# Performance work log

Measured on AMD Instinct MI355X. Metric: run time of the kernel, lower is better.

Reference implementation:

```python
import jax, jax.numpy as jnp
import numpy as np

D_MODEL = 1024
NUM_HEADS = 16
KEY_DIM = 64
VALUE_DIM = 64
NEG_INF = jnp.float32(-1e30)


def setup_inputs() -> dict:
    key = jax.random.key(0)
    ks = jax.random.split(key, 10)
    B, S = 2, 2048
    lim = 1.0 / np.sqrt(D_MODEL)
    x = jax.random.normal(ks[0], (B, S, D_MODEL), dtype=jnp.float32)
    mask = jnp.ones((B, S), dtype=jnp.int32)  # pad mask: 1 = keep
    # stacked per-head linear params (Linear stores weight as [out, in])
    Wq = jax.random.uniform(ks[1], (NUM_HEADS, KEY_DIM, D_MODEL), jnp.float32, -lim, lim)
    bq = jax.random.uniform(ks[2], (NUM_HEADS, KEY_DIM), jnp.float32, -lim, lim)
    Wk = jax.random.uniform(ks[3], (NUM_HEADS, KEY_DIM, D_MODEL), jnp.float32, -lim, lim)
    bk = jax.random.uniform(ks[4], (NUM_HEADS, KEY_DIM), jnp.float32, -lim, lim)
    Wv = jax.random.uniform(ks[5], (NUM_HEADS, VALUE_DIM, D_MODEL), jnp.float32, -lim, lim)
    bv = jax.random.uniform(ks[6], (NUM_HEADS, VALUE_DIM), jnp.float32, -lim, lim)
    lim_o = 1.0 / np.sqrt(NUM_HEADS * VALUE_DIM)
    Wo = jax.random.uniform(ks[7], (D_MODEL, NUM_HEADS * VALUE_DIM), jnp.float32, -lim_o, lim_o)
    bo = jax.random.uniform(ks[8], (D_MODEL,), jnp.float32, -lim_o, lim_o)
    return {"x": x, "mask": mask, "Wq": Wq, "bq": bq, "Wk": Wk, "bk": bk,
            "Wv": Wv, "bv": bv, "Wo": Wo, "bo": bo}


def _mha(x, mask, Wq, bq, Wk, bk, Wv, bv, Wo, bo):
    B, S, _ = x.shape
    # per-head projections: [B, H, S, k]
    q = jnp.einsum('bsd,hkd->bhsk', x, Wq) + bq[None, :, None, :]
    k = jnp.einsum('bsd,hkd->bhsk', x, Wk) + bk[None, :, None, :]
    v = jnp.einsum('bsd,hvd->bhsv', x, Wv) + bv[None, :, None, :]
    scale = 1.0 / np.sqrt(KEY_DIM).astype(np.float32)
    scores = jnp.einsum('bhik,bhjk->bhij', q, k) * scale  # [B, H, S, S]
    # final mask = causal AND pad-row AND pad-col
    causal = jnp.tril(jnp.ones((S, S), dtype=bool))
    pad = mask.astype(bool)
    final = causal[None, None] & pad[:, None, :, None] & pad[:, None, None, :]
    masked = jnp.where(final, scores, NEG_INF)
    w = jax.nn.softmax(masked, axis=-1)
    w = jnp.where(final, w, 0.0)  # fully-masked rows -> zeros, matching loop impl
    out = jnp.einsum('bhij,bhjv->bhiv', w, v)            # [B, H, S, V]
    concat = out.transpose(0, 2, 1, 3).reshape(B, S, NUM_HEADS * VALUE_DIM)
    return concat @ Wo.T + bo


def reference(x, mask, Wq, bq, Wk, bk, Wv, bv, Wo, bo):
    return _mha(x, mask, Wq, bq, Wk, bk, Wv, bv, Wo, bo)
```

## Files before the change

kernel.cpp:

```cpp
#include <hip/hip_runtime.h>

#define SEQ 2048
#define NH 16
#define HD 64
#define DMODEL 1024

__device__ __forceinline__ unsigned int f2bf(float f) {
  unsigned int u = __float_as_uint(f);
  return ((u + 0x7fffu + ((u >> 16) & 1u)) >> 16) & 0xffffu;
}

__device__ __forceinline__ unsigned int pk2bf(float a, float b) {
  unsigned short ua = __builtin_bit_cast(unsigned short, (__bf16)a);
  unsigned short ub = __builtin_bit_cast(unsigned short, (__bf16)b);
  return (unsigned int)ua | ((unsigned int)ub << 16);
}

typedef __bf16 bf16x8 __attribute__((ext_vector_type(8)));
typedef float f32x4 __attribute__((ext_vector_type(4)));

__device__ __forceinline__ void gl2lds16(const unsigned short* g, unsigned short* l) {
  __builtin_amdgcn_global_load_lds(
      (const __attribute__((address_space(1))) unsigned int*)g,
      (__attribute__((address_space(3))) unsigned int*)l, 16, 0, 0);
}

__global__ __launch_bounds__(256) void cast_all_kernel(
    const float* __restrict__ x, const float* __restrict__ wq,
    const float* __restrict__ wk, const float* __restrict__ wv,
    const float* __restrict__ wo,
    unsigned short* __restrict__ xb, unsigned short* __restrict__ wqb,
    unsigned short* __restrict__ wkb, unsigned short* __restrict__ wvb,
    unsigned short* __restrict__ wob) {
  int idx = blockIdx.x * 256 + threadIdx.x;
  if (idx >= 1048576) return;
  const float* src;
  unsigned short* dst;
  int off;
  if (idx < 524288) {
    src = x; dst = xb; off = idx;
  } else {
    int t = idx - 524288;
    int w = t >> 17;
    off = t & 131071;
    src = (w == 0) ? wq : (w == 1) ? wk : (w == 2) ? wv : wo;
    dst = (w == 0) ? wqb : (w == 1) ? wkb : (w == 2) ? wvb : wob;
  }
  const float4* p = reinterpret_cast<const float4*>(src) + (size_t)off * 2;
  float4 a = p[0], b = p[1];
  uint4 o;
  o.x = f2bf(a.x) | (f2bf(a.y) << 16);
  o.y = f2bf(a.z) | (f2bf(a.w) << 16);
  o.z = f2bf(b.x) | (f2bf(b.y) << 16);
  o.w = f2bf(b.z) | (f2bf(b.w) << 16);
  reinterpret_cast<uint4*>(dst)[idx == off ? off : off] = o;
}

template <int MODE>
__global__ __launch_bounds__(256) void gemm128(
    const unsigned short* __restrict__ A, const unsigned short* __restrict__ B,
    const float* __restrict__ bias0, const float* __restrict__ bias1,
    const float* __restrict__ bias2, float* __restrict__ Cf,
    unsigned short* __restrict__ Qo, unsigned short* __restrict__ Ko,
    unsigned short* __restrict__ Vto, int Kdim) {
  __shared__ __align__(16) unsigned short As[128 * 64];
  __shared__ __align__(16) unsigned short Bs[128 * 64];
  const int tid = threadIdx.x;
  const int wave = tid >> 6, lane = tid & 63;
  const int wm = wave >> 1, wn = wave & 1;
  const int fr = lane & 15, quad = lane >> 4;
  const int fx = fr & 7;
  const int n0 = blockIdx.x * 128, m0 = blockIdx.y * 128;

  const int srowg = lane >> 3;
  const int schunk = (lane & 7) ^ (srowg & 7);
  const unsigned short* Abase =
      A + (size_t)(m0 + wave * 32 + srowg) * Kdim + schunk * 8;
  const unsigned short* Bbase =
      B + (size_t)(n0 + wave * 32 + srowg) * Kdim + schunk * 8;
  unsigned short* AsW = As + (wave * 32) * 64;
  unsigned short* BsW = Bs + (wave * 32) * 64;

  f32x4 acc[4][4];
#pragma unroll
  for (int mt = 0; mt < 4; ++mt)
#pragma unroll
    for (int nt = 0; nt < 4; ++nt) acc[mt][nt] = f32x4{0.f, 0.f, 0.f, 0.f};

  for (int k0 = 0; k0 < Kdim; k0 += 64) {
#pragma unroll
    for (int t = 0; t < 4; ++t) {
      gl2lds16(Abase + (size_t)(t * 8) * Kdim + k0, AsW + t * 8 * 64);
      gl2lds16(Bbase + (size_t)(t * 8) * Kdim + k0, BsW + t * 8 * 64);
    }
    __syncthreads();
#pragma unroll
    for (int ks = 0; ks < 2; ++ks) {
      bf16x8 af[4], bfv[4];
#pragma unroll
      for (int mt = 0; mt < 4; ++mt)
        af[mt] = *reinterpret_cast<const bf16x8*>(
            As + (wm * 64 + mt * 16 + fr) * 64 + ((ks * 4 + quad) ^ fx) * 8);
#pragma unroll
      for (int nt = 0; nt < 4; ++nt)
        bfv[nt] = *reinterpret_cast<const bf16x8*>(
            Bs + (wn * 64 + nt * 16 + fr) * 64 + ((ks * 4 + quad) ^ fx) * 8);
#pragma unroll
      for (int mt = 0; mt < 4; ++mt)
#pragma unroll
        for (int nt = 0; nt < 4; ++nt)
          acc[mt][nt] = __builtin_amdgcn_mfma_f32_16x16x32_bf16(
              af[mt], bfv[nt], acc[mt][nt], 0, 0, 0);
    }
    __syncthreads();
  }

  if (MODE == 0) {
    const int seg = n0 >> 10;
    const float* bp = (seg == 0) ? bias0 : (seg == 1) ? bias1 : bias2;
    const float scale = (seg == 0) ? 0.1803368809f : 1.0f;
    unsigned short* QK = (seg == 0) ? Qo : Ko;
#pragma unroll
    for (int nt = 0; nt < 4; ++nt) {
      const int c = (n0 + wn * 64 + nt * 16 + fr) & 1023;
      const int h = c >> 6, d = c & 63;
      const float bs = bp[c];
#pragma unroll
      for (int mt = 0; mt < 4; ++mt) {
        const int mbase = m0 + wm * 64 + mt * 16 + quad * 4;
        const int b = mbase >> 11, s0 = mbase & 2047;
        if (seg < 2) {
          unsigned short* dst = QK + (((size_t)(b * NH + h)) * SEQ + s0) * HD + d;
#pragma unroll
          for (int r = 0; r < 4; ++r)
            dst[(size_t)r * HD] = (unsigned short)f2bf((acc[mt][nt][r] + bs) * scale);
        } else {
          uint2 pk;
          pk.x = pk2bf(acc[mt][nt][0] + bs, acc[mt][nt][1] + bs);
          pk.y = pk2bf(acc[mt][nt][2] + bs, acc[mt][nt][3] + bs);
          *reinterpret_cast<uint2*>(
              Vto + (((size_t)(b * NH + h)) * HD + d) * SEQ + s0) = pk;
        }
      }
    }
  } else {
#pragma unroll
    for (int nt = 0; nt < 4; ++nt) {
      const int cg = n0 + wn * 64 + nt * 16 + fr;
      const float bs = bias0[cg];
#pragma unroll
      for (int mt = 0; mt < 4; ++mt) {
        const int mbase = m0 + wm * 64 + mt * 16 + quad * 4;
#pragma unroll
        for (int r = 0; r < 4; ++r)
          Cf[(size_t)(mbase + r) * DMODEL + cg] = acc[mt][nt][r] + bs;
      }
    }
  }
}

__global__ __launch_bounds__(256, 3) void attn_mfma_kernel(
    const unsigned short* __restrict__ Qg, const unsigned short* __restrict__ Kg,
    const unsigned short* __restrict__ Vtg, const int* __restrict__ mask,
    unsigned short* __restrict__ concat) {
  const int g = blockIdx.x >> 5;
  const int bh = blockIdx.x & 31;
  const int b = bh >> 4;
  const int h = bh & 15;
  const int tid = threadIdx.x;
  const int wave = tid >> 6;
  const int lane = tid & 63;
  const int quad = lane >> 4;
  const int fr = lane & 15;
  const int ibA = 31 - g, ibB = g;

  __shared__ unsigned short Ks[64][72];
  __shared__ unsigned short Vts[64][72];
  __shared__ unsigned short Pt[2][4][16][72];
  __shared__ unsigned int tilebad;

  const unsigned short* Qb = Qg + ((size_t)bh * SEQ) * HD;
  const unsigned short* Kb = Kg + ((size_t)bh * SEQ) * HD;
  const unsigned short* Vtb = Vtg + ((size_t)bh * HD) * SEQ;
  const int* maskb = mask + b * SEQ;

  if (tid == 0) tilebad = 0;
  __syncthreads();
  {
    const int4* mp4 = reinterpret_cast<const int4*>(maskb);
    int4 a = mp4[tid * 2], c = mp4[tid * 2 + 1];
    if (!(a.x && a.y && a.z && a.w && c.x && c.y && c.z && c.w))
      atomicOr(&tilebad, 1u << (tid >> 3));
  }
  __syncthreads();
  const unsigned int tbad = tilebad;

  const int irA = ibA * 64 + wave * 16 + fr;
  const int irB = ibB * 64 + wave * 16 + fr;
  const bf16x8 qA0 = *reinterpret_cast<const bf16x8*>(Qb + (size_t)irA * HD + quad * 8);
  const bf16x8 qA1 = *reinterpret_cast<const bf16x8*>(Qb + (size_t)irA * HD + quad * 8 + 32);
  const bf16x8 qB0 = *reinterpret_cast<const bf16x8*>(Qb + (size_t)irB * HD + quad * 8);
  const bf16x8 qB1 = *reinterpret_cast<const bf16x8*>(Qb + (size_t)irB * HD + quad * 8 + 32);
  const int padA = maskb[irA], padB = maskb[irB];

  f32x4 oA[4], oB[4];
#pragma unroll
  for (int vt = 0; vt < 4; ++vt) { oA[vt] = f32x4{0,0,0,0}; oB[vt] = f32x4{0,0,0,0}; }
  float mA = -1e20f, lA = 0.f, mB = -1e20f, lB = 0.f;

  const int srow = tid >> 2;
  const int spart = (tid & 3) * 2;

  for (int jc = 0; jc <= ibA; ++jc) {
    const int j0 = jc * 64;
    {
      const uint4* kg = reinterpret_cast<const uint4*>(Kb + (size_t)(j0 + srow) * HD);
      const uint4* vg = reinterpret_cast<const uint4*>(Vtb + (size_t)srow * SEQ + j0);
      uint4 ka = kg[spart], kc = kg[spart + 1];
      uint4 va = vg[spart], vc = vg[spart + 1];
      *reinterpret_cast<uint4*>(&Ks[srow][spart * 8]) = ka;
      *reinterpret_cast<uint4*>(&Ks[srow][spart * 8 + 8]) = kc;
      *reinterpret_cast<uint4*>(&Vts[srow][spart * 8]) = va;
      *reinterpret_cast<uint4*>(&Vts[srow][spart * 8 + 8]) = vc;
    }
    __syncthreads();

    const bool doB = (jc <= ibB);
    const bool diagA = (jc == ibA), diagB = (jc == ibB);
    const bool tb = (tbad >> jc) & 1u;

    f32x4 stA[4], stB[4];
#pragma unroll
    for (int jt = 0; jt < 4; ++jt) {
      bf16x8 ka0 = *reinterpret_cast<const bf16x8*>(&Ks[jt * 16 + fr][quad * 8]);
      bf16x8 ka1 = *reinterpret_cast<const bf16x8*>(&Ks[jt * 16 + fr][quad * 8 + 32]);
      stA[jt] = f32x4{0,0,0,0};
      stA[jt] = __builtin_amdgcn_mfma_f32_16x16x32_bf16(ka0, qA0, stA[jt], 0, 0, 0);
      stA[jt] = __builtin_amdgcn_mfma_f32_16x16x32_bf16(ka1, qA1, stA[jt], 0, 0, 0);
      if (doB) {
        stB[jt] = f32x4{0,0,0,0};
        stB[jt] = __builtin_amdgcn_mfma_f32_16x16x32_bf16(ka0, qB0, stB[jt], 0, 0, 0);
        stB[jt] = __builtin_amdgcn_mfma_f32_16x16x32_bf16(ka1, qB1, stB[jt], 0, 0, 0);
      }
    }

    if (tb) {
      const int4* mp = reinterpret_cast<const int4*>(maskb + j0);
#pragma unroll
      for (int jt = 0; jt < 4; ++jt) {
        const int4 mv = mp[jt * 4 + quad];
        if (mv.x == 0) { stA[jt][0] = -1e30f; if (doB) stB[jt][0] = -1e30f; }
        if (mv.y == 0) { stA[jt][1] = -1e30f; if (doB) stB[jt][1] = -1e30f; }
        if (mv.z == 0) { stA[jt][2] = -1e30f; if (doB) stB[jt][2] = -1e30f; }
        if (mv.w == 0) { stA[jt][3] = -1e30f; if (doB) stB[jt][3] = -1e30f; }
      }
    }
    if (diagA) {
#pragma unroll
      for (int jt = 0; jt < 4; ++jt) {
        const int jb = j0 + jt * 16 + quad * 4;
#pragma unroll
        for (int r = 0; r < 4; ++r)
          if (jb + r > irA) stA[jt][r] = -1e30f;
      }
    }
    if (doB && diagB) {
#pragma unroll
      for (int jt = 0; jt < 4; ++jt) {
        const int jb = j0 + jt * 16 + quad * 4;
#pragma unroll
        for (int r = 0; r < 4; ++r)
          if (jb + r > irB) stB[jt][r] = -1e30f;
      }
    }

    {
      float tmax = -1e30f;
#pragma unroll
      for (int jt = 0; jt < 4; ++jt)
#pragma unroll
        for (int r = 0; r < 4; ++r) tmax = fmaxf(tmax, stA[jt][r]);
      tmax = fmaxf(tmax, __shfl_xor(tmax, 16));
      tmax = fmaxf(tmax, __shfl_xor(tmax, 32));
      const bool upd = __ballot(tmax > mA) != 0ull;
      float corr = 1.f;
      if (upd) { const float mn = fmaxf(mA, tmax); corr = __builtin_amdgcn_exp2f(mA - mn); mA = mn; }
      float lloc = 0.f;
#pragma unroll
      for (int jt = 0; jt < 4; ++jt) {
        float p0 = __builtin_amdgcn_exp2f(stA[jt][0] - mA);
        float p1 = __builtin_amdgcn_exp2f(stA[jt][1] - mA);
        float p2 = __builtin_amdgcn_exp2f(stA[jt][2] - mA);
        float p3 = __builtin_amdgcn_exp2f(stA[jt][3] - mA);
        lloc += (p0 + p1) + (p2 + p3);
        uint2 pk; pk.x = pk2bf(p0, p1); pk.y = pk2bf(p2, p3);
        *reinterpret_cast<uint2*>(&Pt[0][wave][fr][jt * 16 + quad * 4]) = pk;
      }
      lloc += __shfl_xor(lloc, 16);
      lloc += __shfl_xor(lloc, 32);
      if (upd) {
        lA = lA * corr + lloc;
#pragma unroll
        for (int vt = 0; vt < 4; ++vt) {
          oA[vt][0] *= corr; oA[vt][1] *= corr; oA[vt][2] *= corr; oA[vt][3] *= corr;
        }
      } else lA += lloc;
    }
    if (doB) {
      float tmax = -1e30f;
#pragma unroll
      for (int jt = 0; jt < 4; ++jt)
#pragma unroll
        for (int r = 0; r < 4; ++r) tmax = fmaxf(tmax, stB[jt][r]);
      tmax = fmaxf(tmax, __shfl_xor(tmax, 16));
      tmax = fmaxf(tmax, __shfl_xor(tmax, 32));
      const bool upd = __ballot(tmax > mB) != 0ull;
      float corr = 1.f;
      if (upd) { const float mn = fmaxf(mB, tmax); corr = __builtin_amdgcn_exp2f(mB - mn); mB = mn; }
      float lloc = 0.f;
#pragma unroll
      for (int jt = 0; jt < 4; ++jt) {
        float p0 = __builtin_amdgcn_exp2f(stB[jt][0] - mB);
        float p1 = __builtin_amdgcn_exp2f(stB[jt][1] - mB);
        float p2 = __builtin_amdgcn_exp2f(stB[jt][2] - mB);
        float p3 = __builtin_amdgcn_exp2f(stB[jt][3] - mB);
        lloc += (p0 + p1) + (p2 + p3);
        uint2 pk; pk.x = pk2bf(p0, p1); pk.y = pk2bf(p2, p3);
        *reinterpret_cast<uint2*>(&Pt[1][wave][fr][jt * 16 + quad * 4]) = pk;
      }
      lloc += __shfl_xor(lloc, 16);
      lloc += __shfl_xor(lloc, 32);
      if (upd) {
        lB = lB * corr + lloc;
#pragma unroll
        for (int vt = 0; vt < 4; ++vt) {
          oB[vt][0] *= corr; oB[vt][1] *= corr; oB[vt][2] *= corr; oB[vt][3] *= corr;
        }
      } else lB += lloc;
    }

    bf16x8 paA0 = *reinterpret_cast<const bf16x8*>(&Pt[0][wave][fr][quad * 8]);
    bf16x8 paA1 = *reinterpret_cast<const bf16x8*>(&Pt[0][wave][fr][quad * 8 + 32]);
    bf16x8 paB0, paB1;
    if (doB) {
      paB0 = *reinterpret_cast<const bf16x8*>(&Pt[1][wave][fr][quad * 8]);
      paB1 = *reinterpret_cast<const bf16x8*>(&Pt[1][wave][fr][quad * 8 + 32]);
    }
#pragma unroll
    for (int vt = 0; vt < 4; ++vt) {
      bf16x8 vb0 = *reinterpret_cast<const bf16x8*>(&Vts[vt * 16 + fr][quad * 8]);
      bf16x8 vb1 = *reinterpret_cast<const bf16x8*>(&Vts[vt * 16 + fr][quad * 8 + 32]);
      oA[vt] = __builtin_amdgcn_mfma_f32_16x16x32_bf16(vb0, paA0, oA[vt], 0, 0, 0);
      oA[vt] = __builtin_amdgcn_mfma_f32_16x16x32_bf16(vb1, paA1, oA[vt], 0, 0, 0);
      if (doB) {
        oB[vt] = __builtin_amdgcn_mfma_f32_16x16x32_bf16(vb0, paB0, oB[vt], 0, 0, 0);
        oB[vt] = __builtin_amdgcn_mfma_f32_16x16x32_bf16(vb1, paB1, oB[vt], 0, 0, 0);
      }
    }
    __syncthreads();
  }

  {
    const float inv = (padA != 0 && lA > 0.f) ? 1.f / lA : 0.f;
    unsigned short* orow = concat + ((size_t)(b * SEQ + irA)) * DMODEL + h * HD;
#pragma unroll
    for (int vt = 0; vt < 4; ++vt) {
      uint2 pk;
      pk.x = pk2bf(oA[vt][0] * inv, oA[vt][1] * inv);
      pk.y = pk2bf(oA[vt][2] * inv, oA[vt][3] * inv);
      *reinterpret_cast<uint2*>(orow + vt * 16 + quad * 4) = pk;
    }
  }
  {
    const float inv = (padB != 0 && lB > 0.f) ? 1.f / lB : 0.f;
    unsigned short* orow = concat + ((size_t)(b * SEQ + irB)) * DMODEL + h * HD;
#pragma unroll
    for (int vt = 0; vt < 4; ++vt) {
      uint2 pk;
      pk.x = pk2bf(oB[vt][0] * inv, oB[vt][1] * inv);
      pk.y = pk2bf(oB[vt][2] * inv, oB[vt][3] * inv);
      *reinterpret_cast<uint2*>(orow + vt * 16 + quad * 4) = pk;
    }
  }
}

extern "C" void kernel_launch(void* const* d_in, const int* in_sizes, int n_in,
                              void* d_out, int out_size, void* d_ws, size_t ws_size,
                              hipStream_t stream) {
  (void)in_sizes; (void)n_in; (void)out_size;
  const float* x  = (const float*)d_in[0];
  const int* mask = (const int*)d_in[1];
  const float* Wq = (const float*)d_in[2];
  const float* bq = (const float*)d_in[3];
  const float* Wk = (const float*)d_in[4];
  const float* bk = (const float*)d_in[5];
  const float* Wv = (const float*)d_in[6];
  const float* bv = (const float*)d_in[7];
  const float* Wo = (const float*)d_in[8];
  const float* bo = (const float*)d_in[9];
  float* out = (float*)d_out;

  char* ws = (char*)d_ws;
  if (ws_size < (48ull << 20)) return;
  unsigned short* xb  = (unsigned short*)(ws);
  unsigned short* wqb = (unsigned short*)(ws + (8ull  << 20));
  unsigned short* wkb = (unsigned short*)(ws + (10ull << 20));
  unsigned short* wvb = (unsigned short*)(ws + (12ull << 20));
  unsigned short* wob = (unsigned short*)(ws + (14ull << 20));
  unsigned short* Qb  = (unsigned short*)(ws + (16ull << 20));
  unsigned short* Kb  = (unsigned short*)(ws + (24ull << 20));
  unsigned short* Vtb = (unsigned short*)(ws + (32ull << 20));
  unsigned short* cb  = (unsigned short*)(ws + (40ull << 20));

  cast_all_kernel<<<4096, 256, 0, stream>>>(x, Wq, Wk, Wv, Wo, xb, wqb, wkb, wvb, wob);

  gemm128<0><<<dim3(24, 32), 256, 0, stream>>>(xb, wqb, bq, bk, bv,
                                               nullptr, Qb, Kb, Vtb, 1024);

  attn_mfma_kernel<<<512, 256, 0, stream>>>(Qb, Kb, Vtb, mask, cb);

  gemm128<1><<<dim3(8, 32), 256, 0, stream>>>(cb, wob, bo, nullptr, nullptr,
                                              out, nullptr, nullptr, nullptr, 1024);
}
```

Before: 200.6 us.

## Split attention blocks into 2-wave CTAs with direct global-to-LDS swizzled K/V loads

The attention kernel now runs 1024 blocks of 128 threads, each handling two 16-row strips instead of four. This doubles the block count and cuts shared memory per block, which should improve occupancy and load balance. K and V tiles are loaded with global_load_lds (one wave for K, one for V) into an XOR-swizzled unpadded layout to avoid bank conflicts without going through registers. The pad-mask bitmap is built with a wave ballot instead of shared atomics and extra barriers. In exchange, each K/V tile is now loaded twice as often across blocks, and every block waits on a single wave's load latency.

Result: no change. 201.9 us (+0.6%).

```diff
diff --git a/kernel.cpp b/kernel.cpp
--- a/kernel.cpp
+++ b/kernel.cpp
@@ -53,7 +53,7 @@
   o.y = f2bf(a.z) | (f2bf(a.w) << 16);
   o.z = f2bf(b.x) | (f2bf(b.y) << 16);
   o.w = f2bf(b.z) | (f2bf(b.w) << 16);
-  reinterpret_cast<uint4*>(dst)[idx == off ? off : off] = o;
+  reinterpret_cast<uint4*>(dst)[off] = o;
 }
 
 template <int MODE>
@@ -159,44 +159,42 @@
   }
 }
 
-__global__ __launch_bounds__(256, 3) void attn_mfma_kernel(
+__global__ __launch_bounds__(128) void attn_mfma_kernel(
     const unsigned short* __restrict__ Qg, const unsigned short* __restrict__ Kg,
     const unsigned short* __restrict__ Vtg, const int* __restrict__ mask,
     unsigned short* __restrict__ concat) {
-  const int g = blockIdx.x >> 5;
+  const int gs = blockIdx.x >> 5;
+  const int g = gs >> 1, sub = gs & 1;
   const int bh = blockIdx.x & 31;
-  const int b = bh >> 4;
-  const int h = bh & 15;
+  const int b = bh >> 4, h = bh & 15;
   const int tid = threadIdx.x;
-  const int wave = tid >> 6;
-  const int lane = tid & 63;
-  const int quad = lane >> 4;
-  const int fr = lane & 15;
+  const int wave = tid >> 6, lane = tid & 63;
+  const int quad = lane >> 4, fr = lane & 15;
+  const int strip = sub * 2 + wave;
   const int ibA = 31 - g, ibB = g;
 
-  __shared__ unsigned short Ks[64][72];
-  __shared__ unsigned short Vts[64][72];
-  __shared__ unsigned short Pt[2][4][16][72];
-  __shared__ unsigned int tilebad;
+  __shared__ __align__(16) unsigned short Ks[64 * 64];
+  __shared__ __align__(16) unsigned short Vts[64 * 64];
+  __shared__ unsigned short Pt[2][2][16][72];
 
   const unsigned short* Qb = Qg + ((size_t)bh * SEQ) * HD;
   const unsigned short* Kb = Kg + ((size_t)bh * SEQ) * HD;
   const unsigned short* Vtb = Vtg + ((size_t)bh * HD) * SEQ;
   const int* maskb = mask + b * SEQ;
 
-  if (tid == 0) tilebad = 0;
-  __syncthreads();
+  bool badl = false;
   {
     const int4* mp4 = reinterpret_cast<const int4*>(maskb);
-    int4 a = mp4[tid * 2], c = mp4[tid * 2 + 1];
-    if (!(a.x && a.y && a.z && a.w && c.x && c.y && c.z && c.w))
-      atomicOr(&tilebad, 1u << (tid >> 3));
-  }
-  __syncthreads();
-  const unsigned int tbad = tilebad;
-
-  const int irA = ibA * 64 + wave * 16 + fr;
-  const int irB = ibB * 64 + wave * 16 + fr;
+#pragma unroll
+    for (int u = 0; u < 8; ++u) {
+      int4 v = mp4[lane * 8 + u];
+      badl |= !(v.x && v.y && v.z && v.w);
+    }
+  }
+  const unsigned long long bm = __ballot(badl);
+
+  const int irA = ibA * 64 + strip * 16 + fr;
+  const int irB = ibB * 64 + strip * 16 + fr;
   const bf16x8 qA0 = *reinterpret_cast<const bf16x8*>(Qb + (size_t)irA * HD + quad * 8);
   const bf16x8 qA1 = *reinterpret_cast<const bf16x8*>(Qb + (size_t)irA * HD + quad * 8 + 32);
   const bf16x8 qB0 = *reinterpret_cast<const bf16x8*>(Qb + (size_t)irB * HD + quad * 8);
@@ -208,32 +206,34 @@
   for (int vt = 0; vt < 4; ++vt) { oA[vt] = f32x4{0,0,0,0}; oB[vt] = f32x4{0,0,0,0}; }
   float mA = -1e20f, lA = 0.f, mB = -1e20f, lB = 0.f;
 
-  const int srow = tid >> 2;
-  const int spart = (tid & 3) * 2;
+  const int srowg = lane >> 3;
+  const int schunk = (lane & 7) ^ (srowg & 7);
+  const unsigned short* Ksrc = Kb + (size_t)srowg * HD + schunk * 8;
+  const unsigned short* Vsrc = Vtb + (size_t)srowg * SEQ + schunk * 8;
+  const int cA0 = (quad ^ (fr & 7)) * 8;
+  const int cA1 = ((quad + 4) ^ (fr & 7)) * 8;
 
   for (int jc = 0; jc <= ibA; ++jc) {
     const int j0 = jc * 64;
-    {
-      const uint4* kg = reinterpret_cast<const uint4*>(Kb + (size_t)(j0 + srow) * HD);
-      const uint4* vg = reinterpret_cast<const uint4*>(Vtb + (size_t)srow * SEQ + j0);
-      uint4 ka = kg[spart], kc = kg[spart + 1];
-      uint4 va = vg[spart], vc = vg[spart + 1];
-      *reinterpret_cast<uint4*>(&Ks[srow][spart * 8]) = ka;
-      *reinterpret_cast<uint4*>(&Ks[srow][spart * 8 + 8]) = kc;
-      *reinterpret_cast<uint4*>(&Vts[srow][spart * 8]) = va;
-      *reinterpret_cast<uint4*>(&Vts[srow][spart * 8 + 8]) = vc;
+    if (wave == 0) {
+#pragma unroll
+      for (int t = 0; t < 8; ++t)
+        gl2lds16(Ksrc + (size_t)(j0 + t * 8) * HD, Ks + t * 8 * 64);
+    } else {
+#pragma unroll
+      for (int t = 0; t < 8; ++t)
+        gl2lds16(Vsrc + (size_t)(t * 8) * SEQ + j0, Vts + t * 8 * 64);
     }
     __syncthreads();
 
     const bool doB = (jc <= ibB);
-    const bool diagA = (jc == ibA), diagB = (jc == ibB);
-    const bool tb = (tbad >> jc) & 1u;
+    const bool tb = ((bm >> (2 * jc)) & 3ull) != 0ull;
 
     f32x4 stA[4], stB[4];
 #pragma unroll
     for (int jt = 0; jt < 4; ++jt) {
-      bf16x8 ka0 = *reinterpret_cast<const bf16x8*>(&Ks[jt * 16 + fr][quad * 8]);
-      bf16x8 ka1 = *reinterpret_cast<const bf16x8*>(&Ks[jt * 16 + fr][quad * 8 + 32]);
+      bf16x8 ka0 = *reinterpret_cast<const bf16x8*>(&Ks[(jt * 16 + fr) * 64 + cA0]);
+      bf16x8 ka1 = *reinterpret_cast<const bf16x8*>(&Ks[(jt * 16 + fr) * 64 + cA1]);
       stA[jt] = f32x4{0,0,0,0};
       stA[jt] = __builtin_amdgcn_mfma_f32_16x16x32_bf16(ka0, qA0, stA[jt], 0, 0, 0);
       stA[jt] = __builtin_amdgcn_mfma_f32_16x16x32_bf16(ka1, qA1, stA[jt], 0, 0, 0);
@@ -255,7 +255,7 @@
         if (mv.w == 0) { stA[jt][3] = -1e30f; if (doB) stB[jt][3] = -1e30f; }
       }
     }
-    if (diagA) {
+    if (jc == ibA) {
 #pragma unroll
       for (int jt = 0; jt < 4; ++jt) {
         const int jb = j0 + jt * 16 + quad * 4;
@@ -264,7 +264,7 @@
           if (jb + r > irA) stA[jt][r] = -1e30f;
       }
     }
-    if (doB && diagB) {
+    if (doB && jc == ibB) {
 #pragma unroll
       for (int jt = 0; jt < 4; ++jt) {
         const int jb = j0 + jt * 16 + quad * 4;
@@ -294,7 +294,7 @@
         float p3 = __builtin_amdgcn_exp2f(stA[jt][3] - mA);
         lloc += (p0 + p1) + (p2 + p3);
         uint2 pk; pk.x = pk2bf(p0, p1); pk.y = pk2bf(p2, p3);
-        *reinterpret_cast<uint2*>(&Pt[0][wave][fr][jt * 16 + quad * 4]) = pk;
+        *reinterpret_cast<uint2*>(&Pt[wave][0][fr][jt * 16 + quad * 4]) = pk;
       }
       lloc += __shfl_xor(lloc, 16);
       lloc += __shfl_xor(lloc, 32);
@@ -326,7 +326,7 @@
         float p3 = __builtin_amdgcn_exp2f(stB[jt][3] - mB);
         lloc += (p0 + p1) + (p2 + p3);
         uint2 pk; pk.x = pk2bf(p0, p1); pk.y = pk2bf(p2, p3);
-        *reinterpret_cast<uint2*>(&Pt[1][wave][fr][jt * 16 + quad * 4]) = pk;
+        *reinterpret_cast<uint2*>(&Pt[wave][1][fr][jt * 16 + quad * 4]) = pk;
       }
       lloc += __shfl_xor(lloc, 16);
       lloc += __shfl_xor(lloc, 32);
@@ -339,17 +339,17 @@
       } else lB += lloc;
     }
 
-    bf16x8 paA0 = *reinterpret_cast<const bf16x8*>(&Pt[0][wave][fr][quad * 8]);
-    bf16x8 paA1 = *reinterpret_cast<const bf16x8*>(&Pt[0][wave][fr][quad * 8 + 32]);
+    bf16x8 paA0 = *reinterpret_cast<const bf16x8*>(&Pt[wave][0][fr][quad * 8]);
+    bf16x8 paA1 = *reinterpret_cast<const bf16x8*>(&Pt[wave][0][fr][quad * 8 + 32]);
     bf16x8 paB0, paB1;
     if (doB) {
-      paB0 = *reinterpret_cast<const bf16x8*>(&Pt[1][wave][fr][quad * 8]);
-      paB1 = *reinterpret_cast<const bf16x8*>(&Pt[1][wave][fr][quad * 8 + 32]);
+      paB0 = *reinterpret_cast<const bf16x8*>(&Pt[wave][1][fr][quad * 8]);
+      paB1 = *reinterpret_cast<const bf16x8*>(&Pt[wave][1][fr][quad * 8 + 32]);
     }
 #pragma unroll
     for (int vt = 0; vt < 4; ++vt) {
-      bf16x8 vb0 = *reinterpret_cast<const bf16x8*>(&Vts[vt * 16 + fr][quad * 8]);
-      bf16x8 vb1 = *reinterpret_cast<const bf16x8*>(&Vts[vt * 16 + fr][quad * 8 + 32]);
+      bf16x8 vb0 = *reinterpret_cast<const bf16x8*>(&Vts[(vt * 16 + fr) * 64 + cA0]);
+      bf16x8 vb1 = *reinterpret_cast<const bf16x8*>(&Vts[(vt * 16 + fr) * 64 + cA1]);
       oA[vt] = __builtin_amdgcn_mfma_f32_16x16x32_bf16(vb0, paA0, oA[vt], 0, 0, 0);
       oA[vt] = __builtin_amdgcn_mfma_f32_16x16x32_bf16(vb1, paA1, oA[vt], 0, 0, 0);
       if (doB) {
@@ -417,7 +417,7 @@
   gemm128<0><<<dim3(24, 32), 256, 0, stream>>>(xb, wqb, bq, bk, bv,
                                                nullptr, Qb, Kb, Vtb, 1024);
 
-  attn_mfma_kernel<<<512, 256, 0, stream>>>(Qb, Kb, Vtb, mask, cb);
+  attn_mfma_kernel<<<1024, 128, 0, stream>>>(Qb, Kb, Vtb, mask, cb);
 
   gemm128<1><<<dim3(8, 32), 256, 0, stream>>>(cb, wob, bo, nullptr, nullptr,
                                               out, nullptr, nullptr, nullptr, 1024);
```
